# Kernel optimization log

Hardware: AMD Instinct MI355X
Metric: run time of the kernel (lower is better)

## Reference

```python
import jax, jax.numpy as jnp
import numpy as np
from jax import lax

NUM_CLS = 58

def _bsign(a):
    # BNN sign: +1 for a >= 0, -1 otherwise
    return jnp.where(a >= 0, 1.0, -1.0).astype(a.dtype)

def _conv(x, w, stride=1):
    return lax.conv_general_dilated(
        x, w, window_strides=(stride, stride), padding='VALID',
        dimension_numbers=('NCHW', 'OIHW', 'NCHW'))

def _binconv(x, w):
    # BinaryConv2d: binarize activations and weights via sign, then conv
    return _conv(_bsign(x), _bsign(w))

def _maxpool(x, k=2, s=2):
    return lax.reduce_window(x, -jnp.inf, lax.max,
                             (1, 1, k, k), (1, 1, s, s), 'VALID')

def setup_inputs() -> dict:
    key = jax.random.key(0)
    ks = jax.random.split(key, 7)
    B = 1024
    x = jax.random.normal(ks[0], (B, 3, 32, 32), dtype=jnp.float32)
    w0 = jax.random.normal(ks[1], (128, 3, 3, 3), dtype=jnp.float32) * 0.1   # float conv
    w1 = jax.random.normal(ks[2], (128, 128, 3, 3), dtype=jnp.float32) * 0.1 # binary conv
    w2 = jax.random.normal(ks[3], (128, 128, 3, 3), dtype=jnp.float32) * 0.1 # binary conv
    w3 = jax.random.normal(ks[4], (128, 128, 3, 3), dtype=jnp.float32) * 0.1 # binary conv
    w4 = jax.random.normal(ks[5], (128, 128, 1, 1), dtype=jnp.float32) * 0.1 # binary 1x1
    w5 = jax.random.normal(ks[6], (NUM_CLS, 128, 1, 1), dtype=jnp.float32) * 0.1  # float 1x1
    return {'x': x, 'w0': w0, 'w1': w1, 'w2': w2, 'w3': w3, 'w4': w4, 'w5': w5}

def reference(x, w0, w1, w2, w3, w4, w5):
    # features
    h = _conv(x, w0)            # [B,128,30,30]
    h = _maxpool(h, 2, 2)       # [B,128,15,15]
    h = _binconv(h, w1)         # [B,128,13,13]
    h = _maxpool(h, 2, 2)       # [B,128,6,6]
    h = _binconv(h, w2)         # [B,128,4,4]
    h = _maxpool(h, 2, 1)       # [B,128,3,3]
    # classifier
    h = _binconv(h, w3)         # [B,128,1,1]
    h = _binconv(h, w4)         # [B,128,1,1]
    h = jax.nn.relu(h)
    h = _conv(h, w5)            # [B,58,1,1]
    return jax.nn.softmax(h, axis=1)
```

## Files before the change

### kernel.cpp

```cpp
#include <hip/hip_runtime.h>
#include <cmath>

#define NUM_CLS 58

typedef _Float16 v8h __attribute__((ext_vector_type(8)));
typedef float v4f __attribute__((ext_vector_type(4)));
typedef int v4i __attribute__((ext_vector_type(4)));
union HU { v8h h; uint4 u; };

__global__ __launch_bounds__(256) void prep_all(
    const float* __restrict__ w0, const float* __restrict__ w1,
    const float* __restrict__ w2, const float* __restrict__ w3,
    const float* __restrict__ w4,
    unsigned long long* __restrict__ wb2,
    unsigned long long* __restrict__ wb3, unsigned long long* __restrict__ wb4,
    _Float16* __restrict__ bsig, _Float16* __restrict__ babs,
    uint4* __restrict__ bw1f) {
    int id = blockIdx.x, tid = threadIdx.x;
    int lane = tid & 63, wv = tid >> 6;
    if (id < 256) {
        int layer = id >> 7, oc = id & 127;
        const float* w = layer == 0 ? w2 : w3;
        unsigned long long* o = layer == 0 ? wb2 : wb3;
        __shared__ float s[1152];
        const float* base = w + (size_t)oc * 1152;
        for (int i = tid; i < 1152; i += 256) s[i] = base[i];
        __syncthreads();
        for (int k = wv; k < 9; k += 4) {
            unsigned long long b0 = __ballot(s[lane * 9 + k] >= 0.f);
            unsigned long long b1 = __ballot(s[(lane + 64) * 9 + k] >= 0.f);
            if (lane == 0) { o[(oc * 9 + k) * 2] = b0; o[(oc * 9 + k) * 2 + 1] = b1; }
        }
    } else if (id < 288) {
        int oc = (id - 256) * 4 + wv;
        unsigned long long b0 = __ballot(w4[oc * 128 + lane] >= 0.f);
        unsigned long long b1 = __ballot(w4[oc * 128 + lane + 64] >= 0.f);
        if (lane == 0) { wb4[oc * 2] = b0; wb4[oc * 2 + 1] = b1; }
    } else if (id < 290) {
        int nt = (id - 288) * 4 + wv;
        int n = nt * 16 + (lane & 15);
        int k0 = (lane >> 4) * 8;
#pragma unroll
        for (int j = 0; j < 8; j++) {
            int k = k0 + j;
            float v = (k < 27) ? w0[n * 27 + k] : 0.f;
            bsig[(nt * 64 + lane) * 8 + j] = (_Float16)v;
            babs[(nt * 64 + lane) * 8 + j] = (_Float16)fabsf(v);
        }
    } else {
        int fi = (id - 290) * 256 + tid;
        int tk = fi >> 9;
        int rem = fi & 511;
        int nt = rem >> 6, ln = rem & 63;
        int oc = nt * 16 + (ln & 15);
        int tap = tk >> 1, kk = tk & 1;
        int icb = kk * 64 + (ln >> 4) * 16;
        const float* wp = w1 + (size_t)oc * 1152 + tap;
        unsigned int dd[4];
#pragma unroll
        for (int q = 0; q < 4; ++q) {
            unsigned int v = 0;
#pragma unroll
            for (int j = 0; j < 4; ++j)
                v |= (wp[(icb + q * 4 + j) * 9] >= 0.f ? 0x01u : 0xFFu) << (8 * j);
            dd[q] = v;
        }
        uint4 d; d.x = dd[0]; d.y = dd[1]; d.z = dd[2]; d.w = dd[3];
        bw1f[fi] = d;
    }
}

union UEXP {
    struct {
        _Float16 xh[3172];
        alignas(16) uint4 bfrag[512];
        uint4 bfraga[512];
    } p0;
    unsigned char expb[225 * 128];
};
union BS {
    alignas(16) unsigned long long bits1[450];
    unsigned short sgn1[144 * 8];
};

__global__ __launch_bounds__(256, 4) void fused_net(
    const float* __restrict__ x, const float* __restrict__ w0,
    const _Float16* __restrict__ bsigG, const _Float16* __restrict__ babsG,
    const uint4* __restrict__ bw1f, const unsigned long long* __restrict__ wb2,
    const unsigned long long* __restrict__ wb3, const unsigned long long* __restrict__ wb4,
    const float* __restrict__ w5, float* __restrict__ out) {
    __shared__ UEXP u;
    __shared__ BS bs;
    __shared__ unsigned int lut[16];
    __shared__ alignas(16) unsigned long long bits2[72];
    __shared__ unsigned long long bits3[18];
    __shared__ unsigned long long bits4[2];
    __shared__ float r_s[128];
    __shared__ float l_s[NUM_CLS];
    __shared__ float e_s[NUM_CLS];
    __shared__ unsigned int qcnt;
    __shared__ unsigned int queue[256];

    int b = blockIdx.x;
    int tid = threadIdx.x;
    int lane = tid & 63, wave = tid >> 6;
    const float* xb = x + (size_t)b * 3072;

    if (tid < 16) {
        unsigned int v = 0;
#pragma unroll
        for (int j = 0; j < 4; ++j) v |= (((tid >> j) & 1) ? 0x01u : 0xFFu) << (8 * j);
        lut[tid] = v;
    }

    {
        for (int i = tid; i < 3072; i += 256) {
            int c = i >> 10, rem = i & 1023;
            u.p0.xh[c * 1057 + (rem >> 5) * 33 + (rem & 31)] = (_Float16)xb[i];
        }
        const uint4* bs4 = (const uint4*)bsigG;
        const uint4* ba4 = (const uint4*)babsG;
        for (int i = tid; i < 512; i += 256) { u.p0.bfrag[i] = bs4[i]; u.p0.bfraga[i] = ba4[i]; }
        if (tid == 0) qcnt = 0;

        int k0 = (lane >> 4) * 8;
        int offj[8];
#pragma unroll
        for (int j = 0; j < 8; j++) {
            int k = k0 + j;
            int c = k / 9, r = (k % 9) / 3, q = k % 3;
            offj[j] = c * 1057 + r * 33 + q;
        }
        unsigned short* b1u16 = (unsigned short*)bs.bits1;
        __syncthreads();

        for (int mt = wave; mt < 57; mt += 4) {
            int mg = mt * 16 + (lane & 15);
            int me = mg < 900 ? mg : 899;
            int p = me >> 2, win = me & 3;
            int py = p / 15, px = p - py * 15;
            int base = (py * 2 + (win >> 1)) * 33 + px * 2 + (win & 1);
            v8h a;
#pragma unroll
            for (int j = 0; j < 8; j++)
                a[j] = (k0 + j < 27) ? u.p0.xh[base + offj[j]] : (_Float16)0.f;
            HU ua; ua.h = a;
            ua.u.x &= 0x7FFF7FFFu; ua.u.y &= 0x7FFF7FFFu;
            ua.u.z &= 0x7FFF7FFFu; ua.u.w &= 0x7FFF7FFFu;
            int myp = mt * 4 + (lane >> 4);
#pragma unroll
            for (int nt = 0; nt < 8; nt++) {
                HU bsf; bsf.u = u.p0.bfrag[nt * 64 + lane];
                HU baf; baf.u = u.p0.bfraga[nt * 64 + lane];
                v4f s  = __builtin_amdgcn_mfma_f32_16x16x32_f16(a,    bsf.h, (v4f){0.f,0.f,0.f,0.f}, 0, 0, 0);
                v4f sa = __builtin_amdgcn_mfma_f32_16x16x32_f16(ua.h, baf.h, (v4f){0.f,0.f,0.f,0.f}, 0, 0, 0);
                float bd0 = fmaf(sa[0], 1.1e-3f, 1e-5f);
                float bd1 = fmaf(sa[1], 1.1e-3f, 1e-5f);
                float bd2 = fmaf(sa[2], 1.1e-3f, 1e-5f);
                float bd3 = fmaf(sa[3], 1.1e-3f, 1e-5f);
                unsigned long long mkpos =
                    __ballot(s[0] >= bd0) | __ballot(s[1] >= bd1) |
                    __ballot(s[2] >= bd2) | __ballot(s[3] >= bd3);
                unsigned long long mkunc =
                    (__ballot(fabsf(s[0]) < bd0) | __ballot(fabsf(s[1]) < bd1) |
                     __ballot(fabsf(s[2]) < bd2) | __ballot(fabsf(s[3]) < bd3)) & ~mkpos;
                if ((lane & 15) == 0 && myp < 225)
                    b1u16[myp * 8 + nt] = (unsigned short)(mkpos >> (lane & 48));
                if (__builtin_expect(mkunc != 0ull, 0)) {
                    if (((mkunc >> lane) & 1ull) && myp < 225) {
                        unsigned int qi = atomicAdd(&qcnt, 1u);
                        if (qi < 256) queue[qi] = (unsigned)myp | ((unsigned)(nt * 16 + (lane & 15)) << 8);
                    }
                }
            }
        }
        __syncthreads();
        unsigned int nq = qcnt < 256u ? qcnt : 256u;
        for (unsigned int i = tid; i < nq; i += 256) {
            unsigned int e = queue[i];
            int p = e & 255; int oc = (e >> 8) & 255;
            int py = p / 15, px = p - py * 15;
            bool pos = false;
#pragma unroll
            for (int win = 0; win < 4; win++) {
                int base = (py * 2 + (win >> 1)) * 32 + px * 2 + (win & 1);
                double sd = 0.0;
#pragma unroll
                for (int k = 0; k < 27; k++) {
                    int c = k / 9, r = (k % 9) / 3, q = k % 3;
                    sd += (double)xb[base + c * 1024 + r * 32 + q] * (double)w0[oc * 27 + k];
                }
                pos |= (sd >= 0.0);
            }
            if (pos) atomicOr(&bs.bits1[p * 2 + (oc >> 6)], 1ull << (oc & 63));
        }
    }
    __syncthreads();

    if (tid < 225) {
        ulonglong2 bw = ((const ulonglong2*)bs.bits1)[tid];
        unsigned char* dst = u.expb + tid * 128;
        int sw = (tid & 7) << 4;
#pragma unroll
        for (int c2 = 0; c2 < 2; ++c2) {
            unsigned long long v = c2 ? bw.y : bw.x;
#pragma unroll
            for (int c = 0; c < 4; ++c) {
                uint4 d;
                d.x = lut[(v >> (c * 16 +  0)) & 15];
                d.y = lut[(v >> (c * 16 +  4)) & 15];
                d.z = lut[(v >> (c * 16 +  8)) & 15];
                d.w = lut[(v >> (c * 16 + 12)) & 15];
                *(uint4*)(dst + (((c2 * 4 + c) * 16) ^ sw)) = d;
            }
        }
    }
    __syncthreads();

    {
        int pg_[9];
#pragma unroll
        for (int mt = 0; mt < 9; ++mt) {
            int w = mt * 16 + (lane & 15);
            int wy = w / 12, wx = w - wy * 12;
            pg_[mt] = (wy * 15 + wx) * 128 + ((lane >> 4) << 4);
        }

        for (int pass = 0; pass < 2; ++pass) {
            int nt = wave * 2 + pass;
            v4i acc[9];
#pragma unroll
            for (int mt = 0; mt < 9; ++mt) acc[mt] = (v4i){0, 0, 0, 0};
#pragma unroll 2
            for (int tk = 0; tk < 18; ++tk) {
                int tap = tk >> 1, kk = tk & 1;
                int tapoff = tap + (tap / 3) * 12;
                int tks = tapoff * 128 + kk * 64;
                uint4 bfr = bw1f[(tk * 8 + nt) * 64 + lane];
                v4i bf; bf.x = (int)bfr.x; bf.y = (int)bfr.y; bf.z = (int)bfr.z; bf.w = (int)bfr.w;
#pragma unroll
                for (int mt = 0; mt < 9; ++mt) {
                    int full = pg_[mt] + tks;
                    int addr = full ^ ((full >> 3) & 0x70);
                    v4i af = *(const v4i*)(u.expb + addr);
                    acc[mt] = __builtin_amdgcn_mfma_i32_16x16x64_i8(af, bf, acc[mt], 0, 0, 0);
                }
            }
#pragma unroll
            for (int mt = 0; mt < 9; ++mt) {
#pragma unroll
                for (int r = 0; r < 4; ++r) {
                    unsigned long long mm = __ballot(acc[mt][r] >= 0);
                    if ((lane & 15) == 0)
                        bs.sgn1[(mt * 16 + (lane >> 4) * 4 + r) * 8 + nt] =
                            (unsigned short)(mm >> lane);
                }
            }
        }
    }
    __syncthreads();

    int wave2 = tid >> 6, half = wave2 & 1, pair = wave2 >> 1;
    int oc = half * 64 + lane;

    {
        int idx = oc >> 4, sh = oc & 15;
        for (int p = pair; p < 36; p += 2) {
            int py = p / 6, px = p % 6;
            int w0i = (2 * py) * 12 + 2 * px;
            unsigned v = (unsigned)bs.sgn1[w0i * 8 + idx]        | (unsigned)bs.sgn1[(w0i + 1) * 8 + idx]
                       | (unsigned)bs.sgn1[(w0i + 12) * 8 + idx] | (unsigned)bs.sgn1[(w0i + 13) * 8 + idx];
            unsigned long long m = __ballot(((v >> sh) & 1u) != 0u);
            if (lane == 0) bits2[p * 2 + half] = m;
        }
    }
    __syncthreads();

    {
        unsigned long long wr[18];
#pragma unroll
        for (int j = 0; j < 18; j++) wr[j] = wb2[oc * 18 + j];
        const ulonglong2* b2v = (const ulonglong2*)bits2;
        for (int p = pair; p < 9; p += 2) {
            int py = p / 3, px = p % 3;
            int P4[4];
#pragma unroll
            for (int dy = 0; dy < 2; dy++)
#pragma unroll
                for (int dx = 0; dx < 2; dx++) {
                    int P = 0;
#pragma unroll
                    for (int ky = 0; ky < 3; ky++)
#pragma unroll
                        for (int kx = 0; kx < 3; kx++) {
                            ulonglong2 q = b2v[(py + dy + ky) * 6 + (px + dx + kx)];
                            P += __popcll(q.x ^ wr[(ky * 3 + kx) * 2]);
                            P += __popcll(q.y ^ wr[(ky * 3 + kx) * 2 + 1]);
                        }
                    P4[dy * 2 + dx] = P;
                }
            unsigned long long m = __ballot(P4[0] <= 576) | __ballot(P4[1] <= 576) |
                                   __ballot(P4[2] <= 576) | __ballot(P4[3] <= 576);
            if (lane == 0) bits3[p * 2 + half] = m;
        }
    }
    __syncthreads();

    if (tid < 128) {
        int P = 0;
#pragma unroll
        for (int k = 0; k < 9; k++) {
            P += __popcll(bits3[k * 2] ^ wb3[tid * 18 + k * 2]);
            P += __popcll(bits3[k * 2 + 1] ^ wb3[tid * 18 + k * 2 + 1]);
        }
        unsigned long long m = __ballot(P <= 576);
        if ((tid & 63) == 0) bits4[tid >> 6] = m;
    }
    __syncthreads();
    if (tid < 128) {
        unsigned long long i0 = bits4[0], i1 = bits4[1];
        int v = 128 - 2 * (int)(__popcll(i0 ^ wb4[tid * 2]) + __popcll(i1 ^ wb4[tid * 2 + 1]));
        r_s[tid] = v > 0 ? (float)v : 0.f;
    }
    __syncthreads();
    if (tid < NUM_CLS) {
        float l = 0.f;
#pragma unroll 8
        for (int k = 0; k < 128; k++) l = fmaf(w5[tid * 128 + k], r_s[k], l);
        l_s[tid] = l;
    }
    __syncthreads();
    if (tid < NUM_CLS) {
        float mx = -1e30f;
        for (int k = 0; k < NUM_CLS; k++) mx = fmaxf(mx, l_s[k]);
        e_s[tid] = expf(l_s[tid] - mx);
    }
    __syncthreads();
    if (tid < NUM_CLS) {
        float sum = 0.f;
        for (int k = 0; k < NUM_CLS; k++) sum += e_s[k];
        out[(size_t)b * NUM_CLS + tid] = e_s[tid] / sum;
    }
}

extern "C" void kernel_launch(void* const* d_in, const int* in_sizes, int n_in,
                              void* d_out, int out_size, void* d_ws, size_t ws_size,
                              hipStream_t stream) {
    const float* x  = (const float*)d_in[0];
    const float* w0 = (const float*)d_in[1];
    const float* w1 = (const float*)d_in[2];
    const float* w2 = (const float*)d_in[3];
    const float* w3 = (const float*)d_in[4];
    const float* w4 = (const float*)d_in[5];
    const float* w5 = (const float*)d_in[6];
    float* out = (float*)d_out;

    int B = in_sizes[0] / 3072;

    size_t off = 0;
    auto carve = [&](size_t bytes) {
        void* p = (char*)d_ws + off;
        off += (bytes + 255) & ~(size_t)255;
        return p;
    };
    unsigned long long* wb2 = (unsigned long long*)carve(1152 * 2 * 8);
    unsigned long long* wb3 = (unsigned long long*)carve(1152 * 2 * 8);
    unsigned long long* wb4 = (unsigned long long*)carve(128 * 2 * 8);
    _Float16* bsig = (_Float16*)carve(8 * 64 * 8 * 2);
    _Float16* babs = (_Float16*)carve(8 * 64 * 8 * 2);
    uint4* bw1f = (uint4*)carve(18 * 8 * 64 * 16);
    (void)ws_size; (void)n_in; (void)out_size;

    prep_all<<<326, 256, 0, stream>>>(w0, w1, w2, w3, w4, wb2, wb3, wb4, bsig, babs, bw1f);
    fused_net<<<B, 256, 0, stream>>>(x, w0, bsig, babs, bw1f, wb2, wb3, wb4, w5, out);
}
```

Baseline: 142.9 us.

## Derive abs weight fragments in-register and reuse A fragments across two N tiles

The kernel stops staging a separate absolute-value weight fragment array in shared memory and instead computes it by masking the sign bits of the loaded signed fragment. This drops one global load and one shared-memory buffer per block. The layer-1 binary conv loop is restructured so each A fragment loaded from shared memory feeds MFMAs for both N tiles at once, with the M tiles split into groups of 5 and 4 to bound register use. This halves A-fragment LDS reads, but raises accumulator register pressure, which could affect occupancy at 4 blocks per CU.

```diff
diff --git a/kernel.cpp b/kernel.cpp
--- a/kernel.cpp
+++ b/kernel.cpp
@@ -7,6 +7,7 @@
 typedef float v4f __attribute__((ext_vector_type(4)));
 typedef int v4i __attribute__((ext_vector_type(4)));
 union HU { v8h h; uint4 u; };
+template<int N> struct IC { static constexpr int value = N; };
 
 __global__ __launch_bounds__(256) void prep_all(
     const float* __restrict__ w0, const float* __restrict__ w1,
@@ -74,7 +75,6 @@
     struct {
         _Float16 xh[3172];
         alignas(16) uint4 bfrag[512];
-        uint4 bfraga[512];
     } p0;
     unsigned char expb[225 * 128];
 };
@@ -105,6 +105,7 @@
     int tid = threadIdx.x;
     int lane = tid & 63, wave = tid >> 6;
     const float* xb = x + (size_t)b * 3072;
+    (void)babsG;
 
     if (tid < 16) {
         unsigned int v = 0;
@@ -119,8 +120,7 @@
             u.p0.xh[c * 1057 + (rem >> 5) * 33 + (rem & 31)] = (_Float16)xb[i];
         }
         const uint4* bs4 = (const uint4*)bsigG;
-        const uint4* ba4 = (const uint4*)babsG;
-        for (int i = tid; i < 512; i += 256) { u.p0.bfrag[i] = bs4[i]; u.p0.bfraga[i] = ba4[i]; }
+        for (int i = tid; i < 512; i += 256) u.p0.bfrag[i] = bs4[i];
         if (tid == 0) qcnt = 0;
 
         int k0 = (lane >> 4) * 8;
@@ -151,7 +151,9 @@
 #pragma unroll
             for (int nt = 0; nt < 8; nt++) {
                 HU bsf; bsf.u = u.p0.bfrag[nt * 64 + lane];
-                HU baf; baf.u = u.p0.bfraga[nt * 64 + lane];
+                HU baf;
+                baf.u.x = bsf.u.x & 0x7FFF7FFFu; baf.u.y = bsf.u.y & 0x7FFF7FFFu;
+                baf.u.z = bsf.u.z & 0x7FFF7FFFu; baf.u.w = bsf.u.w & 0x7FFF7FFFu;
                 v4f s  = __builtin_amdgcn_mfma_f32_16x16x32_f16(a,    bsf.h, (v4f){0.f,0.f,0.f,0.f}, 0, 0, 0);
                 v4f sa = __builtin_amdgcn_mfma_f32_16x16x32_f16(ua.h, baf.h, (v4f){0.f,0.f,0.f,0.f}, 0, 0, 0);
                 float bd0 = fmaf(sa[0], 1.1e-3f, 1e-5f);
@@ -225,38 +227,49 @@
             int wy = w / 12, wx = w - wy * 12;
             pg_[mt] = (wy * 15 + wx) * 128 + ((lane >> 4) << 4);
         }
-
-        for (int pass = 0; pass < 2; ++pass) {
-            int nt = wave * 2 + pass;
-            v4i acc[9];
-#pragma unroll
-            for (int mt = 0; mt < 9; ++mt) acc[mt] = (v4i){0, 0, 0, 0};
+        int ntA = wave * 2, ntB = wave * 2 + 1;
+
+        auto run_group = [&](auto MT0_C, auto MTN_C) {
+            constexpr int MT0 = MT0_C.value;
+            constexpr int MTN = MTN_C.value;
+            v4i acc0[MTN], acc1[MTN];
+#pragma unroll
+            for (int m = 0; m < MTN; ++m) { acc0[m] = (v4i){0,0,0,0}; acc1[m] = (v4i){0,0,0,0}; }
 #pragma unroll 2
             for (int tk = 0; tk < 18; ++tk) {
                 int tap = tk >> 1, kk = tk & 1;
                 int tapoff = tap + (tap / 3) * 12;
                 int tks = tapoff * 128 + kk * 64;
-                uint4 bfr = bw1f[(tk * 8 + nt) * 64 + lane];
-                v4i bf; bf.x = (int)bfr.x; bf.y = (int)bfr.y; bf.z = (int)bfr.z; bf.w = (int)bfr.w;
-#pragma unroll
-                for (int mt = 0; mt < 9; ++mt) {
-                    int full = pg_[mt] + tks;
+                uint4 br0 = bw1f[(tk * 8 + ntA) * 64 + lane];
+                uint4 br1 = bw1f[(tk * 8 + ntB) * 64 + lane];
+                v4i b0; b0.x = (int)br0.x; b0.y = (int)br0.y; b0.z = (int)br0.z; b0.w = (int)br0.w;
+                v4i b1; b1.x = (int)br1.x; b1.y = (int)br1.y; b1.z = (int)br1.z; b1.w = (int)br1.w;
+#pragma unroll
+                for (int m = 0; m < MTN; ++m) {
+                    int full = pg_[MT0 + m] + tks;
                     int addr = full ^ ((full >> 3) & 0x70);
                     v4i af = *(const v4i*)(u.expb + addr);
-                    acc[mt] = __builtin_amdgcn_mfma_i32_16x16x64_i8(af, bf, acc[mt], 0, 0, 0);
-                }
-            }
-#pragma unroll
-            for (int mt = 0; mt < 9; ++mt) {
+                    acc0[m] = __builtin_amdgcn_mfma_i32_16x16x64_i8(af, b0, acc0[m], 0, 0, 0);
+                    acc1[m] = __builtin_amdgcn_mfma_i32_16x16x64_i8(af, b1, acc1[m], 0, 0, 0);
+                }
+            }
+#pragma unroll
+            for (int m = 0; m < MTN; ++m) {
+                constexpr int MTB = 0;  (void)MTB;
+                int mt = MT0 + m;
 #pragma unroll
                 for (int r = 0; r < 4; ++r) {
-                    unsigned long long mm = __ballot(acc[mt][r] >= 0);
-                    if ((lane & 15) == 0)
-                        bs.sgn1[(mt * 16 + (lane >> 4) * 4 + r) * 8 + nt] =
-                            (unsigned short)(mm >> lane);
-                }
-            }
-        }
+                    unsigned long long m0 = __ballot(acc0[m][r] >= 0);
+                    unsigned long long m1 = __ballot(acc1[m][r] >= 0);
+                    if ((lane & 15) == 0) {
+                        bs.sgn1[(mt * 16 + (lane >> 4) * 4 + r) * 8 + ntA] = (unsigned short)(m0 >> lane);
+                        bs.sgn1[(mt * 16 + (lane >> 4) * 4 + r) * 8 + ntB] = (unsigned short)(m1 >> lane);
+                    }
+                }
+            }
+        };
+        run_group(IC<0>{}, IC<5>{});
+        run_group(IC<5>{}, IC<4>{});
     }
     __syncthreads();
 
```

New measurement: 139.3 us. 2.5% less time.

## Compute binary conv2 with int8 MFMA instead of popcount, derive abs weights in-register

Applied to the files above, without the earlier changes.

Replaces the popcount-based XNOR implementation of the second binary conv with an int8 MFMA path. The pooled sign bits are expanded into a swizzled ±1 byte tile in LDS, and weights are pre-packed into MFMA fragment layout by the prep kernel. The kernel also drops the separate |w0| fragment buffer and builds it by masking sign bits of the loaded weight fragment, which saves LDS and global loads. The cost is an extra expansion pass and sync, in exchange for moving the popcount loops onto matrix units.

```diff
diff --git a/kernel.cpp b/kernel.cpp
--- a/kernel.cpp
+++ b/kernel.cpp
@@ -12,32 +12,29 @@
     const float* __restrict__ w0, const float* __restrict__ w1,
     const float* __restrict__ w2, const float* __restrict__ w3,
     const float* __restrict__ w4,
-    unsigned long long* __restrict__ wb2,
     unsigned long long* __restrict__ wb3, unsigned long long* __restrict__ wb4,
     _Float16* __restrict__ bsig, _Float16* __restrict__ babs,
-    uint4* __restrict__ bw1f) {
+    uint4* __restrict__ bw1f, uint4* __restrict__ bw2f) {
     int id = blockIdx.x, tid = threadIdx.x;
     int lane = tid & 63, wv = tid >> 6;
-    if (id < 256) {
-        int layer = id >> 7, oc = id & 127;
-        const float* w = layer == 0 ? w2 : w3;
-        unsigned long long* o = layer == 0 ? wb2 : wb3;
+    if (id < 128) {
+        int oc = id;
         __shared__ float s[1152];
-        const float* base = w + (size_t)oc * 1152;
+        const float* base = w3 + (size_t)oc * 1152;
         for (int i = tid; i < 1152; i += 256) s[i] = base[i];
         __syncthreads();
         for (int k = wv; k < 9; k += 4) {
             unsigned long long b0 = __ballot(s[lane * 9 + k] >= 0.f);
             unsigned long long b1 = __ballot(s[(lane + 64) * 9 + k] >= 0.f);
-            if (lane == 0) { o[(oc * 9 + k) * 2] = b0; o[(oc * 9 + k) * 2 + 1] = b1; }
-        }
-    } else if (id < 288) {
-        int oc = (id - 256) * 4 + wv;
+            if (lane == 0) { wb3[(oc * 9 + k) * 2] = b0; wb3[(oc * 9 + k) * 2 + 1] = b1; }
+        }
+    } else if (id < 160) {
+        int oc = (id - 128) * 4 + wv;
         unsigned long long b0 = __ballot(w4[oc * 128 + lane] >= 0.f);
         unsigned long long b1 = __ballot(w4[oc * 128 + lane + 64] >= 0.f);
         if (lane == 0) { wb4[oc * 2] = b0; wb4[oc * 2 + 1] = b1; }
-    } else if (id < 290) {
-        int nt = (id - 288) * 4 + wv;
+    } else if (id < 162) {
+        int nt = (id - 160) * 4 + wv;
         int n = nt * 16 + (lane & 15);
         int k0 = (lane >> 4) * 8;
 #pragma unroll
@@ -48,14 +45,17 @@
             babs[(nt * 64 + lane) * 8 + j] = (_Float16)fabsf(v);
         }
     } else {
-        int fi = (id - 290) * 256 + tid;
+        bool isw1 = id < 198;
+        const float* w = isw1 ? w1 : w2;
+        uint4* o = isw1 ? bw1f : bw2f;
+        int fi = (isw1 ? id - 162 : id - 198) * 256 + tid;
         int tk = fi >> 9;
         int rem = fi & 511;
         int nt = rem >> 6, ln = rem & 63;
         int oc = nt * 16 + (ln & 15);
         int tap = tk >> 1, kk = tk & 1;
         int icb = kk * 64 + (ln >> 4) * 16;
-        const float* wp = w1 + (size_t)oc * 1152 + tap;
+        const float* wp = w + (size_t)oc * 1152 + tap;
         unsigned int dd[4];
 #pragma unroll
         for (int q = 0; q < 4; ++q) {
@@ -66,7 +66,7 @@
             dd[q] = v;
         }
         uint4 d; d.x = dd[0]; d.y = dd[1]; d.z = dd[2]; d.w = dd[3];
-        bw1f[fi] = d;
+        o[fi] = d;
     }
 }
 
@@ -74,9 +74,12 @@
     struct {
         _Float16 xh[3172];
         alignas(16) uint4 bfrag[512];
-        uint4 bfraga[512];
     } p0;
     unsigned char expb[225 * 128];
+    struct {
+        alignas(16) unsigned char expb2[36 * 128];
+        unsigned short sgn2[16 * 8];
+    } p2;
 };
 union BS {
     alignas(16) unsigned long long bits1[450];
@@ -86,13 +89,12 @@
 __global__ __launch_bounds__(256, 4) void fused_net(
     const float* __restrict__ x, const float* __restrict__ w0,
     const _Float16* __restrict__ bsigG, const _Float16* __restrict__ babsG,
-    const uint4* __restrict__ bw1f, const unsigned long long* __restrict__ wb2,
+    const uint4* __restrict__ bw1f, const uint4* __restrict__ bw2f,
     const unsigned long long* __restrict__ wb3, const unsigned long long* __restrict__ wb4,
     const float* __restrict__ w5, float* __restrict__ out) {
     __shared__ UEXP u;
     __shared__ BS bs;
     __shared__ unsigned int lut[16];
-    __shared__ alignas(16) unsigned long long bits2[72];
     __shared__ unsigned long long bits3[18];
     __shared__ unsigned long long bits4[2];
     __shared__ float r_s[128];
@@ -105,6 +107,7 @@
     int tid = threadIdx.x;
     int lane = tid & 63, wave = tid >> 6;
     const float* xb = x + (size_t)b * 3072;
+    (void)babsG;
 
     if (tid < 16) {
         unsigned int v = 0;
@@ -119,8 +122,7 @@
             u.p0.xh[c * 1057 + (rem >> 5) * 33 + (rem & 31)] = (_Float16)xb[i];
         }
         const uint4* bs4 = (const uint4*)bsigG;
-        const uint4* ba4 = (const uint4*)babsG;
-        for (int i = tid; i < 512; i += 256) { u.p0.bfrag[i] = bs4[i]; u.p0.bfraga[i] = ba4[i]; }
+        for (int i = tid; i < 512; i += 256) u.p0.bfrag[i] = bs4[i];
         if (tid == 0) qcnt = 0;
 
         int k0 = (lane >> 4) * 8;
@@ -151,7 +153,9 @@
 #pragma unroll
             for (int nt = 0; nt < 8; nt++) {
                 HU bsf; bsf.u = u.p0.bfrag[nt * 64 + lane];
-                HU baf; baf.u = u.p0.bfraga[nt * 64 + lane];
+                HU baf;
+                baf.u.x = bsf.u.x & 0x7FFF7FFFu; baf.u.y = bsf.u.y & 0x7FFF7FFFu;
+                baf.u.z = bsf.u.z & 0x7FFF7FFFu; baf.u.w = bsf.u.w & 0x7FFF7FFFu;
                 v4f s  = __builtin_amdgcn_mfma_f32_16x16x32_f16(a,    bsf.h, (v4f){0.f,0.f,0.f,0.f}, 0, 0, 0);
                 v4f sa = __builtin_amdgcn_mfma_f32_16x16x32_f16(ua.h, baf.h, (v4f){0.f,0.f,0.f,0.f}, 0, 0, 0);
                 float bd0 = fmaf(sa[0], 1.1e-3f, 1e-5f);
@@ -260,48 +264,71 @@
     }
     __syncthreads();
 
-    int wave2 = tid >> 6, half = wave2 & 1, pair = wave2 >> 1;
-    int oc = half * 64 + lane;
+    if (tid < 144) {
+        int cell = tid >> 2, cg = tid & 3;
+        int cy = cell / 6, cx = cell - cy * 6;
+        int w0i = (2 * cy) * 12 + 2 * cx;
+        int g0 = cg * 2, g1 = cg * 2 + 1;
+        unsigned v0 = (unsigned)bs.sgn1[w0i * 8 + g0]        | (unsigned)bs.sgn1[(w0i + 1) * 8 + g0]
+                    | (unsigned)bs.sgn1[(w0i + 12) * 8 + g0] | (unsigned)bs.sgn1[(w0i + 13) * 8 + g0];
+        unsigned v1 = (unsigned)bs.sgn1[w0i * 8 + g1]        | (unsigned)bs.sgn1[(w0i + 1) * 8 + g1]
+                    | (unsigned)bs.sgn1[(w0i + 12) * 8 + g1] | (unsigned)bs.sgn1[(w0i + 13) * 8 + g1];
+        unsigned vv = v0 | (v1 << 16);
+        int sw = (cell & 7) << 4;
+        unsigned char* dst = u.p2.expb2 + cell * 128;
+        uint4 d0, d1;
+        d0.x = lut[vv & 15];         d0.y = lut[(vv >> 4) & 15];
+        d0.z = lut[(vv >> 8) & 15];  d0.w = lut[(vv >> 12) & 15];
+        d1.x = lut[(vv >> 16) & 15]; d1.y = lut[(vv >> 20) & 15];
+        d1.z = lut[(vv >> 24) & 15]; d1.w = lut[(vv >> 28) & 15];
+        *(uint4*)(dst + ((cg * 32) ^ sw)) = d0;
+        *(uint4*)(dst + ((cg * 32 + 16) ^ sw)) = d1;
+    }
+    __syncthreads();
 
     {
-        int idx = oc >> 4, sh = oc & 15;
-        for (int p = pair; p < 36; p += 2) {
-            int py = p / 6, px = p % 6;
-            int w0i = (2 * py) * 12 + 2 * px;
-            unsigned v = (unsigned)bs.sgn1[w0i * 8 + idx]        | (unsigned)bs.sgn1[(w0i + 1) * 8 + idx]
-                       | (unsigned)bs.sgn1[(w0i + 12) * 8 + idx] | (unsigned)bs.sgn1[(w0i + 13) * 8 + idx];
-            unsigned long long m = __ballot(((v >> sh) & 1u) != 0u);
-            if (lane == 0) bits2[p * 2 + half] = m;
-        }
-    }
-    __syncthreads();
-
-    {
-        unsigned long long wr[18];
-#pragma unroll
-        for (int j = 0; j < 18; j++) wr[j] = wb2[oc * 18 + j];
-        const ulonglong2* b2v = (const ulonglong2*)bits2;
-        for (int p = pair; p < 9; p += 2) {
-            int py = p / 3, px = p % 3;
-            int P4[4];
-#pragma unroll
-            for (int dy = 0; dy < 2; dy++)
-#pragma unroll
-                for (int dx = 0; dx < 2; dx++) {
-                    int P = 0;
-#pragma unroll
-                    for (int ky = 0; ky < 3; ky++)
-#pragma unroll
-                        for (int kx = 0; kx < 3; kx++) {
-                            ulonglong2 q = b2v[(py + dy + ky) * 6 + (px + dx + kx)];
-                            P += __popcll(q.x ^ wr[(ky * 3 + kx) * 2]);
-                            P += __popcll(q.y ^ wr[(ky * 3 + kx) * 2 + 1]);
-                        }
-                    P4[dy * 2 + dx] = P;
-                }
-            unsigned long long m = __ballot(P4[0] <= 576) | __ballot(P4[1] <= 576) |
-                                   __ballot(P4[2] <= 576) | __ballot(P4[3] <= 576);
-            if (lane == 0) bits3[p * 2 + half] = m;
+        int m = lane & 15;
+        int y2 = m >> 2, x2 = m & 3;
+        int pg2 = (y2 * 6 + x2) * 128 + ((lane >> 4) << 4);
+        int ntA = wave * 2, ntB = wave * 2 + 1;
+        v4i acc0 = (v4i){0, 0, 0, 0}, acc1 = (v4i){0, 0, 0, 0};
+#pragma unroll 2
+        for (int tk = 0; tk < 18; ++tk) {
+            int tap = tk >> 1, kk = tk & 1;
+            int tapoff2 = (tap / 3) * 6 + (tap % 3);
+            int tks = tapoff2 * 128 + kk * 64;
+            uint4 br0 = bw2f[(tk * 8 + ntA) * 64 + lane];
+            uint4 br1 = bw2f[(tk * 8 + ntB) * 64 + lane];
+            v4i b0; b0.x = (int)br0.x; b0.y = (int)br0.y; b0.z = (int)br0.z; b0.w = (int)br0.w;
+            v4i b1; b1.x = (int)br1.x; b1.y = (int)br1.y; b1.z = (int)br1.z; b1.w = (int)br1.w;
+            int full = pg2 + tks;
+            int addr = full ^ ((full >> 3) & 0x70);
+            v4i af = *(const v4i*)(u.p2.expb2 + addr);
+            acc0 = __builtin_amdgcn_mfma_i32_16x16x64_i8(af, b0, acc0, 0, 0, 0);
+            acc1 = __builtin_amdgcn_mfma_i32_16x16x64_i8(af, b1, acc1, 0, 0, 0);
+        }
+#pragma unroll
+        for (int r = 0; r < 4; ++r) {
+            unsigned long long m0 = __ballot(acc0[r] >= 0);
+            unsigned long long m1 = __ballot(acc1[r] >= 0);
+            if ((lane & 15) == 0) {
+                u.p2.sgn2[(((lane >> 4) * 4 + r)) * 8 + ntA] = (unsigned short)(m0 >> lane);
+                u.p2.sgn2[(((lane >> 4) * 4 + r)) * 8 + ntB] = (unsigned short)(m1 >> lane);
+            }
+        }
+    }
+    __syncthreads();
+
+    if (tid < 128) {
+        int idx = tid >> 4, sh = tid & 15;
+        int half = tid >> 6;
+        for (int p = 0; p < 9; ++p) {
+            int py = p / 3, px = p - py * 3;
+            int m00 = py * 4 + px;
+            unsigned v = (unsigned)u.p2.sgn2[m00 * 8 + idx]       | (unsigned)u.p2.sgn2[(m00 + 1) * 8 + idx]
+                       | (unsigned)u.p2.sgn2[(m00 + 4) * 8 + idx] | (unsigned)u.p2.sgn2[(m00 + 5) * 8 + idx];
+            unsigned long long mm = __ballot(((v >> sh) & 1u) != 0u);
+            if ((tid & 63) == 0) bits3[p * 2 + half] = mm;
         }
     }
     __syncthreads();
@@ -363,14 +390,14 @@
         off += (bytes + 255) & ~(size_t)255;
         return p;
     };
-    unsigned long long* wb2 = (unsigned long long*)carve(1152 * 2 * 8);
     unsigned long long* wb3 = (unsigned long long*)carve(1152 * 2 * 8);
     unsigned long long* wb4 = (unsigned long long*)carve(128 * 2 * 8);
     _Float16* bsig = (_Float16*)carve(8 * 64 * 8 * 2);
     _Float16* babs = (_Float16*)carve(8 * 64 * 8 * 2);
     uint4* bw1f = (uint4*)carve(18 * 8 * 64 * 16);
+    uint4* bw2f = (uint4*)carve(18 * 8 * 64 * 16);
     (void)ws_size; (void)n_in; (void)out_size;
 
-    prep_all<<<326, 256, 0, stream>>>(w0, w1, w2, w3, w4, wb2, wb3, wb4, bsig, babs, bw1f);
-    fused_net<<<B, 256, 0, stream>>>(x, w0, bsig, babs, bw1f, wb2, wb3, wb4, w5, out);
+    prep_all<<<234, 256, 0, stream>>>(w0, w1, w2, w3, w4, wb3, wb4, bsig, babs, bw1f, bw2f);
+    fused_net<<<B, 256, 0, stream>>>(x, w0, bsig, babs, bw1f, bw2f, wb3, wb4, w5, out);
 }
```

New measurement: 132.6 us. -7.2%, faster.
